# Kernel tuning notes

Hardware: AMD Instinct MI355X
Metric: run time of the kernel (lower is better)

## Reference

```python
import jax, jax.numpy as jnp
import numpy as np

N = 50000
E = 800000
IN_C = 128
HID = 16
HEADS = 8
OUT_C = 128
NEG_SLOPE = 0.2
EPS = 1e-16


def setup_inputs() -> dict:
    key = jax.random.key(0)
    ks = jax.random.split(key, 12)
    x = jax.random.normal(ks[0], (N, IN_C), dtype=jnp.float32)
    edge_index = jax.random.randint(ks[1], (2, E), 0, N, dtype=jnp.int32)
    s1 = 1.0 / np.sqrt(IN_C)
    s2 = 1.0 / np.sqrt(HID * HEADS)
    W1 = jax.random.normal(ks[2], (IN_C, HEADS * HID), dtype=jnp.float32) * s1
    att_src1 = jax.random.normal(ks[3], (HEADS, HID), dtype=jnp.float32) * s1
    att_dst1 = jax.random.normal(ks[4], (HEADS, HID), dtype=jnp.float32) * s1
    b1 = jnp.zeros((HEADS * HID,), dtype=jnp.float32)
    W2 = jax.random.normal(ks[5], (HEADS * HID, OUT_C), dtype=jnp.float32) * s2
    att_src2 = jax.random.normal(ks[6], (1, OUT_C), dtype=jnp.float32) * s2
    att_dst2 = jax.random.normal(ks[7], (1, OUT_C), dtype=jnp.float32) * s2
    b2 = jnp.zeros((OUT_C,), dtype=jnp.float32)
    return {"x": x, "edge_index": edge_index, "W1": W1, "att_src1": att_src1,
            "att_dst1": att_dst1, "b1": b1, "W2": W2, "att_src2": att_src2,
            "att_dst2": att_dst2, "b2": b2}


def _add_self_loops(edge_index, n):
    loop = jnp.arange(n, dtype=edge_index.dtype)
    src = jnp.concatenate([edge_index[0], loop])
    dst = jnp.concatenate([edge_index[1], loop])
    return src, dst


def gat_conv(x, src, dst, W, att_src, att_dst, bias, heads, out_c, concat):
    n = x.shape[0]
    h = (x @ W).reshape(n, heads, out_c)          # [N, H, C]
    a_src = jnp.einsum('nhc,hc->nh', h, att_src)  # [N, H]
    a_dst = jnp.einsum('nhc,hc->nh', h, att_dst)
    e = a_src[src] + a_dst[dst]                   # [E', H]
    e = jax.nn.leaky_relu(e, NEG_SLOPE)
    # segment softmax over edges grouped by destination node
    m = jax.ops.segment_max(e, dst, num_segments=n)          # [N, H]
    m = jnp.where(jnp.isfinite(m), m, 0.0)
    ex = jnp.exp(e - m[dst])                                  # [E', H]
    denom = jax.ops.segment_sum(ex, dst, num_segments=n)      # [N, H]
    alpha = ex / (denom[dst] + EPS)                            # [E', H]
    msg = alpha[:, :, None] * h[src]                           # [E', H, C]
    out = jax.ops.segment_sum(msg, dst, num_segments=n)       # [N, H, C]
    if concat:
        out = out.reshape(n, heads * out_c)
    else:
        out = out.mean(axis=1)
    return out + bias


def reference(x, edge_index, W1, att_src1, att_dst1, b1, W2, att_src2, att_dst2, b2):
    src, dst = _add_self_loops(edge_index, N)
    h = gat_conv(x, src, dst, W1, att_src1, att_dst1, b1, HEADS, HID, True)
    h = jax.nn.relu(h)
    # dropout is identity in eval mode
    out = gat_conv(h, src, dst, W2, att_src2, att_dst2, b2, 1, OUT_C, False)
    return out
```

## Files before the change

### kernel.cpp

```cpp
#include <hip/hip_runtime.h>


constexpr int N_NODES = 50000;
constexpr int E_EDGES = 800000;
constexpr int ETOT = E_EDGES + N_NODES;
constexpr float NEG_SLOPE = 0.2f;
constexpr float EPS = 1e-16f;
constexpr int SCAN_BLK = 512;
constexpr int NBLK_SCAN = (N_NODES + SCAN_BLK - 1) / SCAN_BLK;

typedef short bf16x8 __attribute__((ext_vector_type(8)));
typedef float f32x4 __attribute__((ext_vector_type(4)));

__device__ __forceinline__ float lrelu(float x) { return x > 0.f ? x : NEG_SLOPE * x; }
__device__ __forceinline__ ushort f2bf(float f) {
    uint u = __float_as_uint(f);
    return (ushort)((u + 0x7fffu + ((u >> 16) & 1u)) >> 16);
}
__device__ __forceinline__ float bf2f(uint u) { return __uint_as_float(u << 16); }

__device__ __forceinline__ void fma8(float* acc, uint4 p, float w, float& ws) {
    ws += w;
    acc[0] += w * bf2f(p.x & 0xffffu); acc[1] += w * bf2f(p.x >> 16);
    acc[2] += w * bf2f(p.y & 0xffffu); acc[3] += w * bf2f(p.y >> 16);
    acc[4] += w * bf2f(p.z & 0xffffu); acc[5] += w * bf2f(p.z >> 16);
    acc[6] += w * bf2f(p.w & 0xffffu); acc[7] += w * bf2f(p.w >> 16);
}

__global__ __launch_bounds__(256) void zero_counts(uint* cnt16) {
    int i = blockIdx.x * blockDim.x + threadIdx.x;
    if (i < (N_NODES + 1) / 2) cnt16[i] = 0;
}

__global__ __launch_bounds__(256) void count_rank(const int* __restrict__ ei,
                                                  uint* __restrict__ cnt16,
                                                  ushort* __restrict__ rank) {
    int e = blockIdx.x * blockDim.x + threadIdx.x;
    if (e >= ETOT) return;
    int d = (e < E_EDGES) ? ei[E_EDGES + e] : (e - E_EDGES);
    const uint shift = (d & 1) * 16;
    uint old = atomicAdd(&cnt16[d >> 1], 1u << shift);
    rank[e] = (ushort)((old >> shift) & 0xffffu);
}

__device__ __forceinline__ uint cnt_at(const uint* cnt16, int i) {
    return (cnt16[i >> 1] >> ((i & 1) * 16)) & 0xffffu;
}

__global__ __launch_bounds__(SCAN_BLK) void block_sums(const uint* __restrict__ cnt16,
                                                       int* __restrict__ bsum) {
    __shared__ int sm[SCAN_BLK];
    int i = blockIdx.x * SCAN_BLK + threadIdx.x;
    sm[threadIdx.x] = (i < N_NODES) ? (int)cnt_at(cnt16, i) : 0;
    __syncthreads();
    for (int off = SCAN_BLK / 2; off > 0; off >>= 1) {
        if (threadIdx.x < off) sm[threadIdx.x] += sm[threadIdx.x + off];
        __syncthreads();
    }
    if (threadIdx.x == 0) bsum[blockIdx.x] = sm[0];
}

__global__ __launch_bounds__(128) void scan98(int* bsum) {
    __shared__ int sm[128];
    int t = threadIdx.x;
    int v = (t < NBLK_SCAN) ? bsum[t] : 0;
    sm[t] = v;
    __syncthreads();
    for (int off = 1; off < 128; off <<= 1) {
        int x = (t >= off) ? sm[t - off] : 0;
        __syncthreads();
        sm[t] += x;
        __syncthreads();
    }
    if (t < NBLK_SCAN) bsum[t] = sm[t] - v;
}

__global__ __launch_bounds__(SCAN_BLK) void scan_final(const uint* __restrict__ cnt16,
                                                       const int* __restrict__ bsum,
                                                       int* __restrict__ rowptr) {
    __shared__ int sm[SCAN_BLK];
    int i = blockIdx.x * SCAN_BLK + threadIdx.x;
    int v = (i < N_NODES) ? (int)cnt_at(cnt16, i) : 0;
    sm[threadIdx.x] = v;
    __syncthreads();
    for (int off = 1; off < SCAN_BLK; off <<= 1) {
        int t = (threadIdx.x >= off) ? sm[threadIdx.x - off] : 0;
        __syncthreads();
        sm[threadIdx.x] += t;
        __syncthreads();
    }
    if (i < N_NODES) rowptr[i] = bsum[blockIdx.x] + sm[threadIdx.x] - v;
    if (blockIdx.x == 0 && threadIdx.x == 0) rowptr[N_NODES] = ETOT;
}

__global__ __launch_bounds__(256) void scatter_kernel(const int* __restrict__ ei,
                                                      const int* __restrict__ rowptr,
                                                      const ushort* __restrict__ rank,
                                                      int* __restrict__ csrc) {
    int e = blockIdx.x * blockDim.x + threadIdx.x;
    if (e >= ETOT) return;
    int s, d;
    if (e < E_EDGES) { s = ei[e]; d = ei[E_EDGES + e]; }
    else             { s = d = e - E_EDGES; }
    const int pos = rowptr[d] + (int)rank[e];
    __builtin_nontemporal_store(s, &csrc[pos]);
}

__global__ __launch_bounds__(256) void convert_W(const float* __restrict__ W1,
                                                 const float* __restrict__ W2,
                                                 const float* __restrict__ attS2,
                                                 const float* __restrict__ attD2,
                                                 ushort* __restrict__ W1t,
                                                 ushort* __restrict__ W2t,
                                                 float* __restrict__ vs,
                                                 float* __restrict__ vd) {
    const float* W = (blockIdx.x == 0) ? W1 : W2;
    ushort* Wt = (blockIdx.x == 0) ? W1t : W2t;
    const int t = threadIdx.x;
    const int n = t >> 1, k0 = (t & 1) * 64;
    for (int k = 0; k < 64; k += 2) {
        uint lo = f2bf(W[(size_t)(k0 + k) * 128 + n]);
        uint hi = f2bf(W[(size_t)(k0 + k + 1) * 128 + n]);
        *(uint*)&Wt[(size_t)n * 128 + k0 + k] = lo | (hi << 16);
    }
    if (blockIdx.x == 1) {
        const int k = t & 127;
        const float* av = (t < 128) ? attS2 : attD2;
        float* dst = (t < 128) ? vs : vd;
        float s = 0.f;
        for (int c = 0; c < 128; ++c) s += W2[(size_t)k * 128 + c] * av[c];
        dst[k] = s;
    }
}

template <bool BF16IN, bool ATT8>
__global__ __launch_bounds__(256) void mfma_gemm(const void* __restrict__ Xv,
                                                 const ushort* __restrict__ Wt,
                                                 ushort* __restrict__ H,
                                                 const float* __restrict__ attS,
                                                 const float* __restrict__ attD,
                                                 float* __restrict__ aS,
                                                 float* __restrict__ aD,
                                                 int nrows) {
    __shared__ __align__(16) char smem[16384 + 32768];
    ushort* lx = (ushort*)smem;
    ushort* lw = (ushort*)(smem + 16384);
    float*  hs = (float*)smem;

    const int t = threadIdx.x;
    const int r0 = blockIdx.x * 64;

    {
        const int n = t >> 1, half = t & 1;
        const ushort* src = Wt + (size_t)n * 128 + half * 64;
        #pragma unroll
        for (int c = 0; c < 8; ++c) {
            int cx = half * 8 + c;
            uint4 v = *(const uint4*)(src + c * 8);
            *(uint4*)&lw[(n * 16 + (cx ^ (n & 7))) * 8] = v;
        }
    }
    {
        const int r = t >> 2, q = t & 3;
        const int grow = r0 + r;
        const uint4 z = {0, 0, 0, 0};
        #pragma unroll
        for (int cc = 0; cc < 4; ++cc) {
            int cx = q * 4 + cc;
            uint4 packed = z;
            if (grow < nrows) {
                if (BF16IN) {
                    packed = *(const uint4*)((const ushort*)Xv + (size_t)grow * 128 + cx * 8);
                } else {
                    const float* X = (const float*)Xv;
                    const float4 f0 = *(const float4*)(X + (size_t)grow * 128 + cx * 8);
                    const float4 f1 = *(const float4*)(X + (size_t)grow * 128 + cx * 8 + 4);
                    packed.x = (uint)f2bf(f0.x) | ((uint)f2bf(f0.y) << 16);
                    packed.y = (uint)f2bf(f0.z) | ((uint)f2bf(f0.w) << 16);
                    packed.z = (uint)f2bf(f1.x) | ((uint)f2bf(f1.y) << 16);
                    packed.w = (uint)f2bf(f1.z) | ((uint)f2bf(f1.w) << 16);
                }
            }
            *(uint4*)&lx[(r * 16 + (cx ^ (r & 7))) * 8] = packed;
        }
    }
    __syncthreads();

    const int wv = t >> 6, l = t & 63;
    const int row = wv * 16 + (l & 15);
    const int lg = l >> 4;
    f32x4 acc[8] = {};

    #pragma unroll
    for (int kb = 0; kb < 4; ++kb) {
        const int cx = kb * 4 + lg;
        bf16x8 a = *(const bf16x8*)&lx[(row * 16 + (cx ^ (row & 7))) * 8];
        #pragma unroll
        for (int nt = 0; nt < 8; ++nt) {
            const int n = nt * 16 + (l & 15);
            bf16x8 b = *(const bf16x8*)&lw[(n * 16 + (cx ^ (n & 7))) * 8];
            acc[nt] = __builtin_amdgcn_mfma_f32_16x16x32_bf16(a, b, acc[nt], 0, 0, 0);
        }
    }

    #pragma unroll
    for (int reg = 0; reg < 4; ++reg) {
        const int grow = r0 + wv * 16 + lg * 4 + reg;
        if (grow < nrows) {
            #pragma unroll
            for (int nt = 0; nt < 8; ++nt)
                H[(size_t)grow * 128 + nt * 16 + (l & 15)] = f2bf(acc[nt][reg]);
        }
    }

    if (ATT8) {
        __syncthreads();
        #pragma unroll
        for (int reg = 0; reg < 4; ++reg) {
            const int r = wv * 16 + lg * 4 + reg;
            #pragma unroll
            for (int nt = 0; nt < 8; ++nt)
                hs[r * 130 + nt * 16 + (l & 15)] = acc[nt][reg];
        }
        __syncthreads();
        for (int q = t; q < 512; q += 256) {
            const int r = q >> 3, h = q & 7;
            if (r0 + r < nrows) {
                float sv = 0.f, dv = 0.f;
                #pragma unroll
                for (int j = 0; j < 16; ++j) {
                    const float hv = hs[r * 130 + h * 16 + j];
                    sv += hv * attS[h * 16 + j];
                    dv += hv * attD[h * 16 + j];
                }
                aS[(size_t)(r0 + r) * 8 + h] = sv;
                aD[(size_t)(r0 + r) * 8 + h] = dv;
            }
        }
    }
}

__global__ __launch_bounds__(256) void agg8(const int* __restrict__ rowptr,
                                            const int* __restrict__ csrc,
                                            const float* __restrict__ aS,
                                            const float* __restrict__ aD,
                                            const ushort* __restrict__ Hm,
                                            const float* __restrict__ bias,
                                            const float* __restrict__ vs,
                                            const float* __restrict__ vd,
                                            ushort* __restrict__ o1bf,
                                            float* __restrict__ aS2,
                                            float* __restrict__ aD2) {
    __shared__ float wlds[4][512];
    const int wv = threadIdx.x >> 6;
    const int d = blockIdx.x * 4 + wv;
    const int lane = threadIdx.x & 63;
    const int g = lane >> 4, i = lane & 15, hc = i >> 1;
    const int hw = lane & 7;
    const float adh = aD[(size_t)d * 8 + hw];

    const int base = rowptr[d], end = rowptr[d + 1];
    float acc[8] = {0.f, 0.f, 0.f, 0.f, 0.f, 0.f, 0.f, 0.f};
    float ws = 0.f;
    const uint4 zero4 = {0, 0, 0, 0};

    for (int c0 = base; c0 < end; c0 += 64) {
        const int rem = min(64, end - c0);
        const int s_l = (lane < rem) ? csrc[c0 + lane] : 0;

        const int nwc = (rem + 7) >> 3;
        for (int jj = 0; jj < nwc; ++jj) {
            const int j = jj * 8 + (lane >> 3);
            const int sj = __shfl(s_l, j);
            float w = 0.f;
            if (j < rem) w = __expf(lrelu(aS[(size_t)sj * 8 + hw] + adh));
            wlds[wv][j * 8 + hw] = w;
        }

        const int niter = (rem + 3) >> 2;
        int j = g;
        int scur = __shfl(s_l, j);
        uint4 pcur = zero4;
        if (j < rem) pcur = *(const uint4*)(Hm + (size_t)scur * 128 + i * 8);
        for (int tt = 0; tt < niter; ++tt) {
            const int jn = j + 4;
            const int snxt = __shfl(s_l, jn & 63);
            uint4 pnxt = zero4;
            if (jn < rem) pnxt = *(const uint4*)(Hm + (size_t)snxt * 128 + i * 8);
            float w = 0.f;
            if (j < rem) w = wlds[wv][j * 8 + hc];
            fma8(acc, pcur, w, ws);
            pcur = pnxt;
            j = jn;
        }
    }

    #pragma unroll
    for (int k = 0; k < 8; ++k) {
        acc[k] += __shfl_xor(acc[k], 16);
        acc[k] += __shfl_xor(acc[k], 32);
    }
    ws += __shfl_xor(ws, 16);
    ws += __shfl_xor(ws, 32);

    const float inv = 1.f / (ws + EPS);
    float v[8];
    #pragma unroll
    for (int k = 0; k < 8; ++k) v[k] = fmaxf(acc[k] * inv + bias[i * 8 + k], 0.f);

    float ps = 0.f, pd = 0.f;
    #pragma unroll
    for (int k = 0; k < 8; ++k) { ps += v[k] * vs[i * 8 + k]; pd += v[k] * vd[i * 8 + k]; }
    #pragma unroll
    for (int off = 1; off <= 8; off <<= 1) {
        ps += __shfl_xor(ps, off);
        pd += __shfl_xor(pd, off);
    }
    if (lane == 0) { aS2[d] = ps; aD2[d] = pd; }

    if (g == 0) {
        uint4 pk;
        pk.x = (uint)f2bf(v[0]) | ((uint)f2bf(v[1]) << 16);
        pk.y = (uint)f2bf(v[2]) | ((uint)f2bf(v[3]) << 16);
        pk.z = (uint)f2bf(v[4]) | ((uint)f2bf(v[5]) << 16);
        pk.w = (uint)f2bf(v[6]) | ((uint)f2bf(v[7]) << 16);
        *(uint4*)(o1bf + (size_t)d * 128 + i * 8) = pk;
    }
}

__global__ __launch_bounds__(256) void agg1(const int* __restrict__ rowptr,
                                            const int* __restrict__ csrc,
                                            const float* __restrict__ aS,
                                            const float* __restrict__ aD,
                                            const ushort* __restrict__ Hm,
                                            const float* __restrict__ bias,
                                            float* __restrict__ out) {
    const int wv = threadIdx.x >> 6;
    const int d = blockIdx.x * 4 + wv;
    const int lane = threadIdx.x & 63;
    const int g = lane >> 4, i = lane & 15;
    const float ad = aD[d];

    const int base = rowptr[d], end = rowptr[d + 1];
    float acc[8] = {0.f, 0.f, 0.f, 0.f, 0.f, 0.f, 0.f, 0.f};
    float ws = 0.f;
    const uint4 zero4 = {0, 0, 0, 0};

    for (int c0 = base; c0 < end; c0 += 64) {
        const int rem = min(64, end - c0);
        const int s_l = (lane < rem) ? csrc[c0 + lane] : 0;
        const float w_l = (lane < rem) ? __expf(lrelu(aS[s_l] + ad)) : 0.f;

        const int niter = (rem + 3) >> 2;
        int j = g;
        int scur = __shfl(s_l, j);
        float wcur = __shfl(w_l, j);
        uint4 pcur = zero4;
        if (j < rem) pcur = *(const uint4*)(Hm + (size_t)scur * 128 + i * 8);
        for (int tt = 0; tt < niter; ++tt) {
            const int jn = j + 4;
            const int snxt = __shfl(s_l, jn & 63);
            const float wnxt = __shfl(w_l, jn & 63);
            uint4 pnxt = zero4;
            if (jn < rem) pnxt = *(const uint4*)(Hm + (size_t)snxt * 128 + i * 8);
            fma8(acc, pcur, wcur, ws);
            pcur = pnxt;
            wcur = wnxt;
            j = jn;
        }
    }

    #pragma unroll
    for (int k = 0; k < 8; ++k) {
        acc[k] += __shfl_xor(acc[k], 16);
        acc[k] += __shfl_xor(acc[k], 32);
    }
    ws += __shfl_xor(ws, 16);
    ws += __shfl_xor(ws, 32);

    if (g == 0) {
        const float inv = 1.f / (ws + EPS);
        float4 o0, o1v;
        o0.x = acc[0] * inv + bias[i * 8 + 0];
        o0.y = acc[1] * inv + bias[i * 8 + 1];
        o0.z = acc[2] * inv + bias[i * 8 + 2];
        o0.w = acc[3] * inv + bias[i * 8 + 3];
        o1v.x = acc[4] * inv + bias[i * 8 + 4];
        o1v.y = acc[5] * inv + bias[i * 8 + 5];
        o1v.z = acc[6] * inv + bias[i * 8 + 6];
        o1v.w = acc[7] * inv + bias[i * 8 + 7];
        *(float4*)(out + (size_t)d * 128 + i * 8) = o0;
        *(float4*)(out + (size_t)d * 128 + i * 8 + 4) = o1v;
    }
}

extern "C" void kernel_launch(void* const* d_in, const int* in_sizes, int n_in,
                              void* d_out, int out_size, void* d_ws, size_t ws_size,
                              hipStream_t stream) {
    const float* x        = (const float*)d_in[0];
    const int*   ei       = (const int*)  d_in[1];
    const float* W1       = (const float*)d_in[2];
    const float* att_src1 = (const float*)d_in[3];
    const float* att_dst1 = (const float*)d_in[4];
    const float* b1       = (const float*)d_in[5];
    const float* W2       = (const float*)d_in[6];
    const float* att_src2 = (const float*)d_in[7];
    const float* att_dst2 = (const float*)d_in[8];
    const float* b2       = (const float*)d_in[9];
    float* out = (float*)d_out;

    ushort* Hbf  = (ushort*)d_ws;
    ushort* o1bf = Hbf + (size_t)N_NODES * 128;
    float*  aS1  = (float*)(o1bf + (size_t)N_NODES * 128);
    float*  aD1  = aS1 + (size_t)N_NODES * 8;
    float*  aS2  = aD1 + (size_t)N_NODES * 8;
    float*  aD2  = aS2 + N_NODES;
    float*  vs   = aD2 + N_NODES;
    float*  vd   = vs + 128;
    ushort* W1t  = (ushort*)(vd + 128);
    ushort* W2t  = W1t + 128 * 128;
    uint* cnt16  = (uint*)(W2t + 128 * 128);
    int* rowptr  = (int*)(cnt16 + (N_NODES + 1) / 2 + 1);
    int* bsum    = rowptr + N_NODES + 1;
    ushort* rank = (ushort*)(bsum + 128);
    int* csrc    = (int*)(rank + ETOT + 2);

    const int zblk = ((N_NODES + 1) / 2 + 255) / 256;
    const int eblk = (ETOT + 255) / 256;
    const int gemm_blocks = (N_NODES + 63) / 64;
    const int agg_blocks = N_NODES / 4;

    convert_W<<<2, 256, 0, stream>>>(W1, W2, att_src2, att_dst2, W1t, W2t, vs, vd);
    zero_counts<<<zblk, 256, 0, stream>>>(cnt16);
    count_rank<<<eblk, 256, 0, stream>>>(ei, cnt16, rank);
    block_sums<<<NBLK_SCAN, SCAN_BLK, 0, stream>>>(cnt16, bsum);
    scan98<<<1, 128, 0, stream>>>(bsum);
    scan_final<<<NBLK_SCAN, SCAN_BLK, 0, stream>>>(cnt16, bsum, rowptr);
    scatter_kernel<<<eblk, 256, 0, stream>>>(ei, rowptr, rank, csrc);

    mfma_gemm<false, true><<<gemm_blocks, 256, 0, stream>>>(
        x, W1t, Hbf, att_src1, att_dst1, aS1, aD1, N_NODES);
    agg8<<<agg_blocks, 256, 0, stream>>>(
        rowptr, csrc, aS1, aD1, Hbf, b1, vs, vd, o1bf, aS2, aD2);

    mfma_gemm<true, false><<<gemm_blocks, 256, 0, stream>>>(
        o1bf, W2t, Hbf, nullptr, nullptr, nullptr, nullptr, N_NODES);
    agg1<<<agg_blocks, 256, 0, stream>>>(
        rowptr, csrc, aS2, aD2, Hbf, b2, out);
}
```

Before: 208.3 us.

## Split aggregation kernels into column chunks and move layer-2 attention into GEMM

The aggregation kernels now launch four column-chunk grids, and each wave processes one 32-column slice of a destination node, 8 edges per iteration. Edge indices and attention weights are recomputed once per chunk. The layer-2 attention scalars are now computed in the second GEMM from its bf16 input tile instead of in the layer-1 aggregation epilogue. The zero-count kernel is folded into convert_W to save a launch. The finer split is meant to raise parallelism and shrink per-node gathers into a cache-friendlier pattern, at the cost of redundant index loads and exp work across chunks.

```diff
diff --git a/kernel.cpp b/kernel.cpp
--- a/kernel.cpp
+++ b/kernel.cpp
@@ -8,6 +8,7 @@
 constexpr float EPS = 1e-16f;
 constexpr int SCAN_BLK = 512;
 constexpr int NBLK_SCAN = (N_NODES + SCAN_BLK - 1) / SCAN_BLK;
+constexpr int AGG_BPC = 12500;
 
 typedef short bf16x8 __attribute__((ext_vector_type(8)));
 typedef float f32x4 __attribute__((ext_vector_type(4)));
@@ -19,17 +20,37 @@
 }
 __device__ __forceinline__ float bf2f(uint u) { return __uint_as_float(u << 16); }
 
-__device__ __forceinline__ void fma8(float* acc, uint4 p, float w, float& ws) {
-    ws += w;
-    acc[0] += w * bf2f(p.x & 0xffffu); acc[1] += w * bf2f(p.x >> 16);
-    acc[2] += w * bf2f(p.y & 0xffffu); acc[3] += w * bf2f(p.y >> 16);
-    acc[4] += w * bf2f(p.z & 0xffffu); acc[5] += w * bf2f(p.z >> 16);
-    acc[6] += w * bf2f(p.w & 0xffffu); acc[7] += w * bf2f(p.w >> 16);
-}
-
-__global__ __launch_bounds__(256) void zero_counts(uint* cnt16) {
-    int i = blockIdx.x * blockDim.x + threadIdx.x;
-    if (i < (N_NODES + 1) / 2) cnt16[i] = 0;
+__global__ __launch_bounds__(256) void convert_W(const float* __restrict__ W1,
+                                                 const float* __restrict__ W2,
+                                                 const float* __restrict__ attS2,
+                                                 const float* __restrict__ attD2,
+                                                 ushort* __restrict__ W1t,
+                                                 ushort* __restrict__ W2t,
+                                                 float* __restrict__ vs,
+                                                 float* __restrict__ vd,
+                                                 uint* __restrict__ cnt16) {
+    const int t = threadIdx.x;
+    if (blockIdx.x >= 2) {
+        const int i = (blockIdx.x - 2) * 256 + t;
+        if (i < (N_NODES + 1) / 2) cnt16[i] = 0;
+        return;
+    }
+    const float* W = (blockIdx.x == 0) ? W1 : W2;
+    ushort* Wt = (blockIdx.x == 0) ? W1t : W2t;
+    const int n = t >> 1, k0 = (t & 1) * 64;
+    for (int k = 0; k < 64; k += 2) {
+        uint lo = f2bf(W[(size_t)(k0 + k) * 128 + n]);
+        uint hi = f2bf(W[(size_t)(k0 + k + 1) * 128 + n]);
+        *(uint*)&Wt[(size_t)n * 128 + k0 + k] = lo | (hi << 16);
+    }
+    if (blockIdx.x == 1) {
+        const int k = t & 127;
+        const float* av = (t < 128) ? attS2 : attD2;
+        float* dst = (t < 128) ? vs : vd;
+        float s = 0.f;
+        for (int c = 0; c < 128; ++c) s += W2[(size_t)k * 128 + c] * av[c];
+        dst[k] = s;
+    }
 }
 
 __global__ __launch_bounds__(256) void count_rank(const int* __restrict__ ei,
@@ -106,34 +127,7 @@
     __builtin_nontemporal_store(s, &csrc[pos]);
 }
 
-__global__ __launch_bounds__(256) void convert_W(const float* __restrict__ W1,
-                                                 const float* __restrict__ W2,
-                                                 const float* __restrict__ attS2,
-                                                 const float* __restrict__ attD2,
-                                                 ushort* __restrict__ W1t,
-                                                 ushort* __restrict__ W2t,
-                                                 float* __restrict__ vs,
-                                                 float* __restrict__ vd) {
-    const float* W = (blockIdx.x == 0) ? W1 : W2;
-    ushort* Wt = (blockIdx.x == 0) ? W1t : W2t;
-    const int t = threadIdx.x;
-    const int n = t >> 1, k0 = (t & 1) * 64;
-    for (int k = 0; k < 64; k += 2) {
-        uint lo = f2bf(W[(size_t)(k0 + k) * 128 + n]);
-        uint hi = f2bf(W[(size_t)(k0 + k + 1) * 128 + n]);
-        *(uint*)&Wt[(size_t)n * 128 + k0 + k] = lo | (hi << 16);
-    }
-    if (blockIdx.x == 1) {
-        const int k = t & 127;
-        const float* av = (t < 128) ? attS2 : attD2;
-        float* dst = (t < 128) ? vs : vd;
-        float s = 0.f;
-        for (int c = 0; c < 128; ++c) s += W2[(size_t)k * 128 + c] * av[c];
-        dst[k] = s;
-    }
-}
-
-template <bool BF16IN, bool ATT8>
+template <bool BF16IN, bool ATT8, bool ATTIN>
 __global__ __launch_bounds__(256) void mfma_gemm(const void* __restrict__ Xv,
                                                  const ushort* __restrict__ Wt,
                                                  ushort* __restrict__ H,
@@ -238,159 +232,155 @@
             }
         }
     }
-}
-
-__global__ __launch_bounds__(256) void agg8(const int* __restrict__ rowptr,
-                                            const int* __restrict__ csrc,
-                                            const float* __restrict__ aS,
-                                            const float* __restrict__ aD,
-                                            const ushort* __restrict__ Hm,
-                                            const float* __restrict__ bias,
-                                            const float* __restrict__ vs,
-                                            const float* __restrict__ vd,
-                                            ushort* __restrict__ o1bf,
-                                            float* __restrict__ aS2,
-                                            float* __restrict__ aD2) {
-    __shared__ float wlds[4][512];
+
+    if (ATTIN) {
+        const int r = t >> 2, qq = t & 3;
+        float ps = 0.f, pd = 0.f;
+        #pragma unroll
+        for (int cc = 0; cc < 4; ++cc) {
+            const int cx = qq * 4 + cc;
+            const uint4 p = *(const uint4*)&lx[(r * 16 + (cx ^ (r & 7))) * 8];
+            const uint w[4] = {p.x, p.y, p.z, p.w};
+            #pragma unroll
+            for (int q = 0; q < 4; ++q) {
+                const float e0 = bf2f(w[q] & 0xffffu);
+                const float e1 = bf2f(w[q] >> 16);
+                ps += e0 * attS[cx * 8 + 2 * q] + e1 * attS[cx * 8 + 2 * q + 1];
+                pd += e0 * attD[cx * 8 + 2 * q] + e1 * attD[cx * 8 + 2 * q + 1];
+            }
+        }
+        ps += __shfl_xor(ps, 1); ps += __shfl_xor(ps, 2);
+        pd += __shfl_xor(pd, 1); pd += __shfl_xor(pd, 2);
+        if (qq == 0 && r0 + r < nrows) { aS[r0 + r] = ps; aD[r0 + r] = pd; }
+    }
+}
+
+__global__ __launch_bounds__(256) void agg8c(const int* __restrict__ rowptr,
+                                             const int* __restrict__ csrc,
+                                             const float* __restrict__ aS,
+                                             const float* __restrict__ aD,
+                                             const ushort* __restrict__ Hm,
+                                             const float* __restrict__ bias,
+                                             ushort* __restrict__ o1bf) {
+    __shared__ float wlds[4][128];
+    const int bid = blockIdx.x;
+    const int c = bid / AGG_BPC;
+    const int b = bid - c * AGG_BPC;
     const int wv = threadIdx.x >> 6;
-    const int d = blockIdx.x * 4 + wv;
+    const int d = b * 4 + wv;
     const int lane = threadIdx.x & 63;
-    const int g = lane >> 4, i = lane & 15, hc = i >> 1;
-    const int hw = lane & 7;
-    const float adh = aD[(size_t)d * 8 + hw];
+    const int g = lane >> 3, i = lane & 7;
+    const int hh = i >> 2;
+    const int h0 = 2 * c;
+
+    const float ad0 = aD[(size_t)d * 8 + h0];
+    const float ad1 = aD[(size_t)d * 8 + h0 + 1];
 
     const int base = rowptr[d], end = rowptr[d + 1];
-    float acc[8] = {0.f, 0.f, 0.f, 0.f, 0.f, 0.f, 0.f, 0.f};
-    float ws = 0.f;
-    const uint4 zero4 = {0, 0, 0, 0};
+    float acc0 = 0.f, acc1 = 0.f, acc2 = 0.f, acc3 = 0.f, ws = 0.f;
 
     for (int c0 = base; c0 < end; c0 += 64) {
         const int rem = min(64, end - c0);
         const int s_l = (lane < rem) ? csrc[c0 + lane] : 0;
-
-        const int nwc = (rem + 7) >> 3;
-        for (int jj = 0; jj < nwc; ++jj) {
-            const int j = jj * 8 + (lane >> 3);
-            const int sj = __shfl(s_l, j);
-            float w = 0.f;
-            if (j < rem) w = __expf(lrelu(aS[(size_t)sj * 8 + hw] + adh));
-            wlds[wv][j * 8 + hw] = w;
-        }
-
-        const int niter = (rem + 3) >> 2;
-        int j = g;
-        int scur = __shfl(s_l, j);
-        uint4 pcur = zero4;
-        if (j < rem) pcur = *(const uint4*)(Hm + (size_t)scur * 128 + i * 8);
-        for (int tt = 0; tt < niter; ++tt) {
-            const int jn = j + 4;
-            const int snxt = __shfl(s_l, jn & 63);
-            uint4 pnxt = zero4;
-            if (jn < rem) pnxt = *(const uint4*)(Hm + (size_t)snxt * 128 + i * 8);
-            float w = 0.f;
-            if (j < rem) w = wlds[wv][j * 8 + hc];
-            fma8(acc, pcur, w, ws);
-            pcur = pnxt;
-            j = jn;
+        float w0 = 0.f, w1 = 0.f;
+        if (lane < rem) {
+            w0 = __expf(lrelu(aS[(size_t)s_l * 8 + h0] + ad0));
+            w1 = __expf(lrelu(aS[(size_t)s_l * 8 + h0 + 1] + ad1));
+        }
+        wlds[wv][lane * 2 + 0] = w0;
+        wlds[wv][lane * 2 + 1] = w1;
+
+        const int niter = (rem + 7) >> 3;
+        #pragma unroll 2
+        for (int it = 0; it < niter; ++it) {
+            const int j = it * 8 + g;
+            const int s = __shfl(s_l, j);
+            const float wj = wlds[wv][j * 2 + hh];
+            const uint2 p = *(const uint2*)(Hm + (size_t)s * 128 + c * 32 + i * 4);
+            acc0 += wj * bf2f(p.x & 0xffffu);
+            acc1 += wj * bf2f(p.x >> 16);
+            acc2 += wj * bf2f(p.y & 0xffffu);
+            acc3 += wj * bf2f(p.y >> 16);
+            ws += wj;
         }
     }
 
     #pragma unroll
-    for (int k = 0; k < 8; ++k) {
-        acc[k] += __shfl_xor(acc[k], 16);
-        acc[k] += __shfl_xor(acc[k], 32);
-    }
-    ws += __shfl_xor(ws, 16);
-    ws += __shfl_xor(ws, 32);
-
-    const float inv = 1.f / (ws + EPS);
-    float v[8];
-    #pragma unroll
-    for (int k = 0; k < 8; ++k) v[k] = fmaxf(acc[k] * inv + bias[i * 8 + k], 0.f);
-
-    float ps = 0.f, pd = 0.f;
-    #pragma unroll
-    for (int k = 0; k < 8; ++k) { ps += v[k] * vs[i * 8 + k]; pd += v[k] * vd[i * 8 + k]; }
-    #pragma unroll
-    for (int off = 1; off <= 8; off <<= 1) {
-        ps += __shfl_xor(ps, off);
-        pd += __shfl_xor(pd, off);
-    }
-    if (lane == 0) { aS2[d] = ps; aD2[d] = pd; }
+    for (int off = 8; off <= 32; off <<= 1) {
+        acc0 += __shfl_xor(acc0, off); acc1 += __shfl_xor(acc1, off);
+        acc2 += __shfl_xor(acc2, off); acc3 += __shfl_xor(acc3, off);
+        ws   += __shfl_xor(ws,   off);
+    }
 
     if (g == 0) {
-        uint4 pk;
-        pk.x = (uint)f2bf(v[0]) | ((uint)f2bf(v[1]) << 16);
-        pk.y = (uint)f2bf(v[2]) | ((uint)f2bf(v[3]) << 16);
-        pk.z = (uint)f2bf(v[4]) | ((uint)f2bf(v[5]) << 16);
-        pk.w = (uint)f2bf(v[6]) | ((uint)f2bf(v[7]) << 16);
-        *(uint4*)(o1bf + (size_t)d * 128 + i * 8) = pk;
-    }
-}
-
-__global__ __launch_bounds__(256) void agg1(const int* __restrict__ rowptr,
-                                            const int* __restrict__ csrc,
-                                            const float* __restrict__ aS,
-                                            const float* __restrict__ aD,
-                                            const ushort* __restrict__ Hm,
-                                            const float* __restrict__ bias,
-                                            float* __restrict__ out) {
+        const float inv = 1.f / (ws + EPS);
+        const int ch = c * 32 + i * 4;
+        const float v0 = fmaxf(acc0 * inv + bias[ch + 0], 0.f);
+        const float v1 = fmaxf(acc1 * inv + bias[ch + 1], 0.f);
+        const float v2 = fmaxf(acc2 * inv + bias[ch + 2], 0.f);
+        const float v3 = fmaxf(acc3 * inv + bias[ch + 3], 0.f);
+        uint2 pk;
+        pk.x = (uint)f2bf(v0) | ((uint)f2bf(v1) << 16);
+        pk.y = (uint)f2bf(v2) | ((uint)f2bf(v3) << 16);
+        *(uint2*)(o1bf + (size_t)d * 128 + ch) = pk;
+    }
+}
+
+__global__ __launch_bounds__(256) void agg1c(const int* __restrict__ rowptr,
+                                             const int* __restrict__ csrc,
+                                             const float* __restrict__ aS,
+                                             const float* __restrict__ aD,
+                                             const ushort* __restrict__ Hm,
+                                             const float* __restrict__ bias,
+                                             float* __restrict__ out) {
+    const int bid = blockIdx.x;
+    const int c = bid / AGG_BPC;
+    const int b = bid - c * AGG_BPC;
     const int wv = threadIdx.x >> 6;
-    const int d = blockIdx.x * 4 + wv;
+    const int d = b * 4 + wv;
     const int lane = threadIdx.x & 63;
-    const int g = lane >> 4, i = lane & 15;
+    const int g = lane >> 3, i = lane & 7;
     const float ad = aD[d];
 
     const int base = rowptr[d], end = rowptr[d + 1];
-    float acc[8] = {0.f, 0.f, 0.f, 0.f, 0.f, 0.f, 0.f, 0.f};
-    float ws = 0.f;
-    const uint4 zero4 = {0, 0, 0, 0};
+    float acc0 = 0.f, acc1 = 0.f, acc2 = 0.f, acc3 = 0.f, ws = 0.f;
 
     for (int c0 = base; c0 < end; c0 += 64) {
         const int rem = min(64, end - c0);
         const int s_l = (lane < rem) ? csrc[c0 + lane] : 0;
         const float w_l = (lane < rem) ? __expf(lrelu(aS[s_l] + ad)) : 0.f;
 
-        const int niter = (rem + 3) >> 2;
-        int j = g;
-        int scur = __shfl(s_l, j);
-        float wcur = __shfl(w_l, j);
-        uint4 pcur = zero4;
-        if (j < rem) pcur = *(const uint4*)(Hm + (size_t)scur * 128 + i * 8);
-        for (int tt = 0; tt < niter; ++tt) {
-            const int jn = j + 4;
-            const int snxt = __shfl(s_l, jn & 63);
-            const float wnxt = __shfl(w_l, jn & 63);
-            uint4 pnxt = zero4;
-            if (jn < rem) pnxt = *(const uint4*)(Hm + (size_t)snxt * 128 + i * 8);
-            fma8(acc, pcur, wcur, ws);
-            pcur = pnxt;
-            wcur = wnxt;
-            j = jn;
+        const int niter = (rem + 7) >> 3;
+        #pragma unroll 2
+        for (int it = 0; it < niter; ++it) {
+            const int j = it * 8 + g;
+            const int s = __shfl(s_l, j);
+            const float wj = __shfl(w_l, j);
+            const uint2 p = *(const uint2*)(Hm + (size_t)s * 128 + c * 32 + i * 4);
+            acc0 += wj * bf2f(p.x & 0xffffu);
+            acc1 += wj * bf2f(p.x >> 16);
+            acc2 += wj * bf2f(p.y & 0xffffu);
+            acc3 += wj * bf2f(p.y >> 16);
+            ws += wj;
         }
     }
 
     #pragma unroll
-    for (int k = 0; k < 8; ++k) {
-        acc[k] += __shfl_xor(acc[k], 16);
-        acc[k] += __shfl_xor(acc[k], 32);
-    }
-    ws += __shfl_xor(ws, 16);
-    ws += __shfl_xor(ws, 32);
+    for (int off = 8; off <= 32; off <<= 1) {
+        acc0 += __shfl_xor(acc0, off); acc1 += __shfl_xor(acc1, off);
+        acc2 += __shfl_xor(acc2, off); acc3 += __shfl_xor(acc3, off);
+        ws   += __shfl_xor(ws,   off);
+    }
 
     if (g == 0) {
         const float inv = 1.f / (ws + EPS);
-        float4 o0, o1v;
-        o0.x = acc[0] * inv + bias[i * 8 + 0];
-        o0.y = acc[1] * inv + bias[i * 8 + 1];
-        o0.z = acc[2] * inv + bias[i * 8 + 2];
-        o0.w = acc[3] * inv + bias[i * 8 + 3];
-        o1v.x = acc[4] * inv + bias[i * 8 + 4];
-        o1v.y = acc[5] * inv + bias[i * 8 + 5];
-        o1v.z = acc[6] * inv + bias[i * 8 + 6];
-        o1v.w = acc[7] * inv + bias[i * 8 + 7];
-        *(float4*)(out + (size_t)d * 128 + i * 8) = o0;
-        *(float4*)(out + (size_t)d * 128 + i * 8 + 4) = o1v;
+        const int ch = c * 32 + i * 4;
+        float4 o;
+        o.x = acc0 * inv + bias[ch + 0];
+        o.y = acc1 * inv + bias[ch + 1];
+        o.z = acc2 * inv + bias[ch + 2];
+        o.w = acc3 * inv + bias[ch + 3];
+        *(float4*)(out + (size_t)d * 128 + ch) = o;
     }
 }
 
@@ -428,23 +418,21 @@
     const int zblk = ((N_NODES + 1) / 2 + 255) / 256;
     const int eblk = (ETOT + 255) / 256;
     const int gemm_blocks = (N_NODES + 63) / 64;
-    const int agg_blocks = N_NODES / 4;
-
-    convert_W<<<2, 256, 0, stream>>>(W1, W2, att_src2, att_dst2, W1t, W2t, vs, vd);
-    zero_counts<<<zblk, 256, 0, stream>>>(cnt16);
+    const int agg_blocks = 4 * AGG_BPC;
+
+    convert_W<<<2 + zblk, 256, 0, stream>>>(W1, W2, att_src2, att_dst2,
+                                            W1t, W2t, vs, vd, cnt16);
     count_rank<<<eblk, 256, 0, stream>>>(ei, cnt16, rank);
     block_sums<<<NBLK_SCAN, SCAN_BLK, 0, stream>>>(cnt16, bsum);
     scan98<<<1, 128, 0, stream>>>(bsum);
     scan_final<<<NBLK_SCAN, SCAN_BLK, 0, stream>>>(cnt16, bsum, rowptr);
     scatter_kernel<<<eblk, 256, 0, stream>>>(ei, rowptr, rank, csrc);
 
-    mfma_gemm<false, true><<<gemm_blocks, 256, 0, stream>>>(
+    mfma_gemm<false, true, false><<<gemm_blocks, 256, 0, stream>>>(
         x, W1t, Hbf, att_src1, att_dst1, aS1, aD1, N_NODES);
-    agg8<<<agg_blocks, 256, 0, stream>>>(
-        rowptr, csrc, aS1, aD1, Hbf, b1, vs, vd, o1bf, aS2, aD2);
-
-    mfma_gemm<true, false><<<gemm_blocks, 256, 0, stream>>>(
-        o1bf, W2t, Hbf, nullptr, nullptr, nullptr, nullptr, N_NODES);
-    agg1<<<agg_blocks, 256, 0, stream>>>(
-        rowptr, csrc, aS2, aD2, Hbf, b2, out);
-}
+    agg8c<<<agg_blocks, 256, 0, stream>>>(rowptr, csrc, aS1, aD1, Hbf, b1, o1bf);
+
+    mfma_gemm<true, false, true><<<gemm_blocks, 256, 0, stream>>>(
+        o1bf, W2t, Hbf, vs, vd, aS2, aD2, N_NODES);
+    agg1c<<<agg_blocks, 256, 0, stream>>>(rowptr, csrc, aS2, aD2, Hbf, b2, out);
+}
```

Result: slower. 309.6 us (+48.6%).

## Fuse CSR build kernels into GEMM launches and deepen gather prefetch in aggregation

Applied to the files above, without the earlier changes.

Zeroing of the degree counts moves into the weight-conversion launch. The count/rank atomics run as extra blocks of the first GEMM launch, and the two-level scan is merged into one kernel that every block recomputes redundantly. Together these cut the number of kernel launches and let the edge counting overlap the GEMM. The layer-2 attention projections move out of agg8 and into the second GEMM epilogue, which reads the bf16 input tile from LDS. Both aggregation kernels now keep four gathered rows in flight instead of one, to hide gather latency at the cost of more registers.

```diff
diff --git a/kernel.cpp b/kernel.cpp
--- a/kernel.cpp
+++ b/kernel.cpp
@@ -27,20 +27,37 @@
     acc[6] += w * bf2f(p.w & 0xffffu); acc[7] += w * bf2f(p.w >> 16);
 }
 
-__global__ __launch_bounds__(256) void zero_counts(uint* cnt16) {
-    int i = blockIdx.x * blockDim.x + threadIdx.x;
-    if (i < (N_NODES + 1) / 2) cnt16[i] = 0;
-}
-
-__global__ __launch_bounds__(256) void count_rank(const int* __restrict__ ei,
-                                                  uint* __restrict__ cnt16,
-                                                  ushort* __restrict__ rank) {
-    int e = blockIdx.x * blockDim.x + threadIdx.x;
-    if (e >= ETOT) return;
-    int d = (e < E_EDGES) ? ei[E_EDGES + e] : (e - E_EDGES);
-    const uint shift = (d & 1) * 16;
-    uint old = atomicAdd(&cnt16[d >> 1], 1u << shift);
-    rank[e] = (ushort)((old >> shift) & 0xffffu);
+__global__ __launch_bounds__(256) void convert_W(const float* __restrict__ W1,
+                                                 const float* __restrict__ W2,
+                                                 const float* __restrict__ attS2,
+                                                 const float* __restrict__ attD2,
+                                                 ushort* __restrict__ W1t,
+                                                 ushort* __restrict__ W2t,
+                                                 float* __restrict__ vs,
+                                                 float* __restrict__ vd,
+                                                 uint* __restrict__ cnt16) {
+    const int t = threadIdx.x;
+    if (blockIdx.x >= 2) {
+        const int i = (blockIdx.x - 2) * 256 + t;
+        if (i < (N_NODES + 1) / 2) cnt16[i] = 0;
+        return;
+    }
+    const float* W = (blockIdx.x == 0) ? W1 : W2;
+    ushort* Wt = (blockIdx.x == 0) ? W1t : W2t;
+    const int n = t >> 1, k0 = (t & 1) * 64;
+    for (int k = 0; k < 64; k += 2) {
+        uint lo = f2bf(W[(size_t)(k0 + k) * 128 + n]);
+        uint hi = f2bf(W[(size_t)(k0 + k + 1) * 128 + n]);
+        *(uint*)&Wt[(size_t)n * 128 + k0 + k] = lo | (hi << 16);
+    }
+    if (blockIdx.x == 1) {
+        const int k = t & 127;
+        const float* av = (t < 128) ? attS2 : attD2;
+        float* dst = (t < 128) ? vs : vd;
+        float s = 0.f;
+        for (int c = 0; c < 128; ++c) s += W2[(size_t)k * 128 + c] * av[c];
+        dst[k] = s;
+    }
 }
 
 __device__ __forceinline__ uint cnt_at(const uint* cnt16, int i) {
@@ -60,37 +77,36 @@
     if (threadIdx.x == 0) bsum[blockIdx.x] = sm[0];
 }
 
-__global__ __launch_bounds__(128) void scan98(int* bsum) {
-    __shared__ int sm[128];
-    int t = threadIdx.x;
-    int v = (t < NBLK_SCAN) ? bsum[t] : 0;
+__global__ __launch_bounds__(SCAN_BLK) void scan_final_fused(const uint* __restrict__ cnt16,
+                                                             const int* __restrict__ bsum,
+                                                             int* __restrict__ rowptr) {
+    __shared__ int sb[128];
+    __shared__ int sm[SCAN_BLK];
+    const int t = threadIdx.x;
+    if (t < 128) sb[t] = (t < NBLK_SCAN) ? bsum[t] : 0;
+    __syncthreads();
+    for (int off = 1; off < 128; off <<= 1) {
+        int v = 0;
+        if (t < 128 && t >= off) v = sb[t - off];
+        __syncthreads();
+        if (t < 128) sb[t] += v;
+        __syncthreads();
+    }
+    const int bid = blockIdx.x;
+    const int bpre = sb[bid] - bsum[bid];
+
+    const int i = bid * SCAN_BLK + t;
+    const int v = (i < N_NODES) ? (int)cnt_at(cnt16, i) : 0;
     sm[t] = v;
     __syncthreads();
-    for (int off = 1; off < 128; off <<= 1) {
+    for (int off = 1; off < SCAN_BLK; off <<= 1) {
         int x = (t >= off) ? sm[t - off] : 0;
         __syncthreads();
         sm[t] += x;
         __syncthreads();
     }
-    if (t < NBLK_SCAN) bsum[t] = sm[t] - v;
-}
-
-__global__ __launch_bounds__(SCAN_BLK) void scan_final(const uint* __restrict__ cnt16,
-                                                       const int* __restrict__ bsum,
-                                                       int* __restrict__ rowptr) {
-    __shared__ int sm[SCAN_BLK];
-    int i = blockIdx.x * SCAN_BLK + threadIdx.x;
-    int v = (i < N_NODES) ? (int)cnt_at(cnt16, i) : 0;
-    sm[threadIdx.x] = v;
-    __syncthreads();
-    for (int off = 1; off < SCAN_BLK; off <<= 1) {
-        int t = (threadIdx.x >= off) ? sm[threadIdx.x - off] : 0;
-        __syncthreads();
-        sm[threadIdx.x] += t;
-        __syncthreads();
-    }
-    if (i < N_NODES) rowptr[i] = bsum[blockIdx.x] + sm[threadIdx.x] - v;
-    if (blockIdx.x == 0 && threadIdx.x == 0) rowptr[N_NODES] = ETOT;
+    if (i < N_NODES) rowptr[i] = bpre + sm[t] - v;
+    if (bid == 0 && t == 0) rowptr[N_NODES] = ETOT;
 }
 
 __global__ __launch_bounds__(256) void scatter_kernel(const int* __restrict__ ei,
@@ -106,34 +122,7 @@
     __builtin_nontemporal_store(s, &csrc[pos]);
 }
 
-__global__ __launch_bounds__(256) void convert_W(const float* __restrict__ W1,
-                                                 const float* __restrict__ W2,
-                                                 const float* __restrict__ attS2,
-                                                 const float* __restrict__ attD2,
-                                                 ushort* __restrict__ W1t,
-                                                 ushort* __restrict__ W2t,
-                                                 float* __restrict__ vs,
-                                                 float* __restrict__ vd) {
-    const float* W = (blockIdx.x == 0) ? W1 : W2;
-    ushort* Wt = (blockIdx.x == 0) ? W1t : W2t;
-    const int t = threadIdx.x;
-    const int n = t >> 1, k0 = (t & 1) * 64;
-    for (int k = 0; k < 64; k += 2) {
-        uint lo = f2bf(W[(size_t)(k0 + k) * 128 + n]);
-        uint hi = f2bf(W[(size_t)(k0 + k + 1) * 128 + n]);
-        *(uint*)&Wt[(size_t)n * 128 + k0 + k] = lo | (hi << 16);
-    }
-    if (blockIdx.x == 1) {
-        const int k = t & 127;
-        const float* av = (t < 128) ? attS2 : attD2;
-        float* dst = (t < 128) ? vs : vd;
-        float s = 0.f;
-        for (int c = 0; c < 128; ++c) s += W2[(size_t)k * 128 + c] * av[c];
-        dst[k] = s;
-    }
-}
-
-template <bool BF16IN, bool ATT8>
+template <bool BF16IN, bool ATT8, bool ATTIN>
 __global__ __launch_bounds__(256) void mfma_gemm(const void* __restrict__ Xv,
                                                  const ushort* __restrict__ Wt,
                                                  ushort* __restrict__ H,
@@ -141,14 +130,29 @@
                                                  const float* __restrict__ attD,
                                                  float* __restrict__ aS,
                                                  float* __restrict__ aD,
-                                                 int nrows) {
+                                                 const int* __restrict__ ei,
+                                                 uint* __restrict__ cnt16,
+                                                 ushort* __restrict__ rank,
+                                                 int cblocks, int nrows) {
     __shared__ __align__(16) char smem[16384 + 32768];
     ushort* lx = (ushort*)smem;
     ushort* lw = (ushort*)(smem + 16384);
     float*  hs = (float*)smem;
 
     const int t = threadIdx.x;
-    const int r0 = blockIdx.x * 64;
+
+    if (blockIdx.x < cblocks) {
+        const int e = blockIdx.x * 256 + t;
+        if (e < ETOT) {
+            const int d = (e < E_EDGES) ? ei[E_EDGES + e] : (e - E_EDGES);
+            const uint shift = (d & 1) * 16;
+            const uint old = atomicAdd(&cnt16[d >> 1], 1u << shift);
+            rank[e] = (ushort)((old >> shift) & 0xffffu);
+        }
+        return;
+    }
+
+    const int r0 = (blockIdx.x - cblocks) * 64;
 
     {
         const int n = t >> 1, half = t & 1;
@@ -238,7 +242,36 @@
             }
         }
     }
-}
+
+    if (ATTIN) {
+        const int r = t >> 2, qq = t & 3;
+        float ps = 0.f, pd = 0.f;
+        #pragma unroll
+        for (int cc = 0; cc < 4; ++cc) {
+            const int cx = qq * 4 + cc;
+            const uint4 p = *(const uint4*)&lx[(r * 16 + (cx ^ (r & 7))) * 8];
+            const uint w[4] = {p.x, p.y, p.z, p.w};
+            #pragma unroll
+            for (int q = 0; q < 4; ++q) {
+                const float e0 = bf2f(w[q] & 0xffffu);
+                const float e1 = bf2f(w[q] >> 16);
+                ps += e0 * attS[cx * 8 + 2 * q] + e1 * attS[cx * 8 + 2 * q + 1];
+                pd += e0 * attD[cx * 8 + 2 * q] + e1 * attD[cx * 8 + 2 * q + 1];
+            }
+        }
+        ps += __shfl_xor(ps, 1); ps += __shfl_xor(ps, 2);
+        pd += __shfl_xor(pd, 1); pd += __shfl_xor(pd, 2);
+        if (qq == 0 && r0 + r < nrows) { aS[r0 + r] = ps; aD[r0 + r] = pd; }
+    }
+}
+
+#define GISSUE(P, JJ)                                                          \
+    {                                                                          \
+        const int jx_ = (JJ);                                                  \
+        const int sx_ = __shfl(s_l, jx_ & 63);                                 \
+        P = zero4;                                                             \
+        if (jx_ < rem) P = *(const uint4*)(Hm + (size_t)sx_ * 128 + i * 8);    \
+    }
 
 __global__ __launch_bounds__(256) void agg8(const int* __restrict__ rowptr,
                                             const int* __restrict__ csrc,
@@ -246,11 +279,7 @@
                                             const float* __restrict__ aD,
                                             const ushort* __restrict__ Hm,
                                             const float* __restrict__ bias,
-                                            const float* __restrict__ vs,
-                                            const float* __restrict__ vd,
-                                            ushort* __restrict__ o1bf,
-                                            float* __restrict__ aS2,
-                                            float* __restrict__ aD2) {
+                                            ushort* __restrict__ o1bf) {
     __shared__ float wlds[4][512];
     const int wv = threadIdx.x >> 6;
     const int d = blockIdx.x * 4 + wv;
@@ -268,30 +297,44 @@
         const int rem = min(64, end - c0);
         const int s_l = (lane < rem) ? csrc[c0 + lane] : 0;
 
+        uint4 p0, p1, p2, p3;
+        GISSUE(p0, g); GISSUE(p1, g + 4); GISSUE(p2, g + 8); GISSUE(p3, g + 12);
+
         const int nwc = (rem + 7) >> 3;
         for (int jj = 0; jj < nwc; ++jj) {
             const int j = jj * 8 + (lane >> 3);
-            const int sj = __shfl(s_l, j);
+            const int sj = __shfl(s_l, j & 63);
             float w = 0.f;
             if (j < rem) w = __expf(lrelu(aS[(size_t)sj * 8 + hw] + adh));
             wlds[wv][j * 8 + hw] = w;
         }
 
         const int niter = (rem + 3) >> 2;
-        int j = g;
-        int scur = __shfl(s_l, j);
-        uint4 pcur = zero4;
-        if (j < rem) pcur = *(const uint4*)(Hm + (size_t)scur * 128 + i * 8);
-        for (int tt = 0; tt < niter; ++tt) {
-            const int jn = j + 4;
-            const int snxt = __shfl(s_l, jn & 63);
-            uint4 pnxt = zero4;
-            if (jn < rem) pnxt = *(const uint4*)(Hm + (size_t)snxt * 128 + i * 8);
-            float w = 0.f;
-            if (j < rem) w = wlds[wv][j * 8 + hc];
-            fma8(acc, pcur, w, ws);
-            pcur = pnxt;
-            j = jn;
+        for (int tb = 0; tb < niter; tb += 4) {
+            const int j0 = 4 * tb + g;
+            {
+                const float w = (j0 < rem) ? wlds[wv][j0 * 8 + hc] : 0.f;
+                fma8(acc, p0, w, ws);
+                GISSUE(p0, j0 + 16);
+            }
+            {
+                const int j1 = j0 + 4;
+                const float w = (j1 < rem) ? wlds[wv][j1 * 8 + hc] : 0.f;
+                fma8(acc, p1, w, ws);
+                GISSUE(p1, j1 + 16);
+            }
+            {
+                const int j2 = j0 + 8;
+                const float w = (j2 < rem) ? wlds[wv][j2 * 8 + hc] : 0.f;
+                fma8(acc, p2, w, ws);
+                GISSUE(p2, j2 + 16);
+            }
+            {
+                const int j3 = j0 + 12;
+                const float w = (j3 < rem) ? wlds[wv][j3 * 8 + hc] : 0.f;
+                fma8(acc, p3, w, ws);
+                GISSUE(p3, j3 + 16);
+            }
         }
     }
 
@@ -303,22 +346,11 @@
     ws += __shfl_xor(ws, 16);
     ws += __shfl_xor(ws, 32);
 
-    const float inv = 1.f / (ws + EPS);
-    float v[8];
-    #pragma unroll
-    for (int k = 0; k < 8; ++k) v[k] = fmaxf(acc[k] * inv + bias[i * 8 + k], 0.f);
-
-    float ps = 0.f, pd = 0.f;
-    #pragma unroll
-    for (int k = 0; k < 8; ++k) { ps += v[k] * vs[i * 8 + k]; pd += v[k] * vd[i * 8 + k]; }
-    #pragma unroll
-    for (int off = 1; off <= 8; off <<= 1) {
-        ps += __shfl_xor(ps, off);
-        pd += __shfl_xor(pd, off);
-    }
-    if (lane == 0) { aS2[d] = ps; aD2[d] = pd; }
-
     if (g == 0) {
+        const float inv = 1.f / (ws + EPS);
+        float v[8];
+        #pragma unroll
+        for (int k = 0; k < 8; ++k) v[k] = fmaxf(acc[k] * inv + bias[i * 8 + k], 0.f);
         uint4 pk;
         pk.x = (uint)f2bf(v[0]) | ((uint)f2bf(v[1]) << 16);
         pk.y = (uint)f2bf(v[2]) | ((uint)f2bf(v[3]) << 16);
@@ -349,24 +381,42 @@
     for (int c0 = base; c0 < end; c0 += 64) {
         const int rem = min(64, end - c0);
         const int s_l = (lane < rem) ? csrc[c0 + lane] : 0;
+
+        uint4 p0, p1, p2, p3;
+        GISSUE(p0, g); GISSUE(p1, g + 4); GISSUE(p2, g + 8); GISSUE(p3, g + 12);
+
         const float w_l = (lane < rem) ? __expf(lrelu(aS[s_l] + ad)) : 0.f;
 
         const int niter = (rem + 3) >> 2;
-        int j = g;
-        int scur = __shfl(s_l, j);
-        float wcur = __shfl(w_l, j);
-        uint4 pcur = zero4;
-        if (j < rem) pcur = *(const uint4*)(Hm + (size_t)scur * 128 + i * 8);
-        for (int tt = 0; tt < niter; ++tt) {
-            const int jn = j + 4;
-            const int snxt = __shfl(s_l, jn & 63);
-            const float wnxt = __shfl(w_l, jn & 63);
-            uint4 pnxt = zero4;
-            if (jn < rem) pnxt = *(const uint4*)(Hm + (size_t)snxt * 128 + i * 8);
-            fma8(acc, pcur, wcur, ws);
-            pcur = pnxt;
-            wcur = wnxt;
-            j = jn;
+        for (int tb = 0; tb < niter; tb += 4) {
+            const int j0 = 4 * tb + g;
+            {
+                const float wr = __shfl(w_l, j0 & 63);
+                const float w = (j0 < rem) ? wr : 0.f;
+                fma8(acc, p0, w, ws);
+                GISSUE(p0, j0 + 16);
+            }
+            {
+                const int j1 = j0 + 4;
+                const float wr = __shfl(w_l, j1 & 63);
+                const float w = (j1 < rem) ? wr : 0.f;
+                fma8(acc, p1, w, ws);
+                GISSUE(p1, j1 + 16);
+            }
+            {
+                const int j2 = j0 + 8;
+                const float wr = __shfl(w_l, j2 & 63);
+                const float w = (j2 < rem) ? wr : 0.f;
+                fma8(acc, p2, w, ws);
+                GISSUE(p2, j2 + 16);
+            }
+            {
+                const int j3 = j0 + 12;
+                const float wr = __shfl(w_l, j3 & 63);
+                const float w = (j3 < rem) ? wr : 0.f;
+                fma8(acc, p3, w, ws);
+                GISSUE(p3, j3 + 16);
+            }
         }
     }
 
@@ -430,21 +480,20 @@
     const int gemm_blocks = (N_NODES + 63) / 64;
     const int agg_blocks = N_NODES / 4;
 
-    convert_W<<<2, 256, 0, stream>>>(W1, W2, att_src2, att_dst2, W1t, W2t, vs, vd);
-    zero_counts<<<zblk, 256, 0, stream>>>(cnt16);
-    count_rank<<<eblk, 256, 0, stream>>>(ei, cnt16, rank);
+    convert_W<<<2 + zblk, 256, 0, stream>>>(W1, W2, att_src2, att_dst2,
+                                            W1t, W2t, vs, vd, cnt16);
+
+    mfma_gemm<false, true, false><<<eblk + gemm_blocks, 256, 0, stream>>>(
+        x, W1t, Hbf, att_src1, att_dst1, aS1, aD1, ei, cnt16, rank, eblk, N_NODES);
+
     block_sums<<<NBLK_SCAN, SCAN_BLK, 0, stream>>>(cnt16, bsum);
-    scan98<<<1, 128, 0, stream>>>(bsum);
-    scan_final<<<NBLK_SCAN, SCAN_BLK, 0, stream>>>(cnt16, bsum, rowptr);
+    scan_final_fused<<<NBLK_SCAN, SCAN_BLK, 0, stream>>>(cnt16, bsum, rowptr);
     scatter_kernel<<<eblk, 256, 0, stream>>>(ei, rowptr, rank, csrc);
 
-    mfma_gemm<false, true><<<gemm_blocks, 256, 0, stream>>>(
-        x, W1t, Hbf, att_src1, att_dst1, aS1, aD1, N_NODES);
-    agg8<<<agg_blocks, 256, 0, stream>>>(
-        rowptr, csrc, aS1, aD1, Hbf, b1, vs, vd, o1bf, aS2, aD2);
-
-    mfma_gemm<true, false><<<gemm_blocks, 256, 0, stream>>>(
-        o1bf, W2t, Hbf, nullptr, nullptr, nullptr, nullptr, N_NODES);
-    agg1<<<agg_blocks, 256, 0, stream>>>(
-        rowptr, csrc, aS2, aD2, Hbf, b2, out);
-}
+    agg8<<<agg_blocks, 256, 0, stream>>>(rowptr, csrc, aS1, aD1, Hbf, b1, o1bf);
+
+    mfma_gemm<true, false, true><<<gemm_blocks, 256, 0, stream>>>(
+        o1bf, W2t, Hbf, vs, vd, aS2, aD2, nullptr, nullptr, nullptr, 0, N_NODES);
+
+    agg1<<<agg_blocks, 256, 0, stream>>>(rowptr, csrc, aS2, aD2, Hbf, b2, out);
+}
```

Result: slower. 216.6 us (+4.0%).
